# Kernel tuning notes

Hardware: AMD Instinct MI355X
Metric: run time of the kernel (lower is better)

## Reference

```python
import jax, jax.numpy as jnp
import numpy as np

V, D, NH, T_MAX, L, MLP = 50257, 1024, 16, 1024, 12, 4
HD = D // NH
F = D * MLP
B, T = 2, 1024


def setup_inputs() -> dict:
    key = jax.random.key(0)
    ks = jax.random.split(key, 16)
    s = 0.02
    inp = {
        'tokens': jax.random.randint(ks[0], (B, T), 0, V, dtype=jnp.int32),
        'wte': jax.random.normal(ks[1], (V, D), jnp.float32) * s,
        'wpe': jax.random.normal(ks[2], (T_MAX, D), jnp.float32) * s,
        'ln1_w': jnp.ones((L, D)), 'ln1_b': jnp.zeros((L, D)),
        'attn_w': jax.random.normal(ks[3], (L, D, 3 * D), jnp.float32) * s,
        'attn_b': jnp.zeros((L, 3 * D)),
        'aproj_w': jax.random.normal(ks[4], (L, D, D), jnp.float32) * s,
        'aproj_b': jnp.zeros((L, D)),
        'ln2_w': jnp.ones((L, D)), 'ln2_b': jnp.zeros((L, D)),
        'fc_w': jax.random.normal(ks[5], (L, D, F), jnp.float32) * s,
        'fc_b': jnp.zeros((L, F)),
        'proj_w': jax.random.normal(ks[6], (L, F, D), jnp.float32) * s,
        'proj_b': jnp.zeros((L, D)),
        'lnf_w': jnp.ones((D,)), 'lnf_b': jnp.zeros((D,)),
    }
    return inp


def _ln(x, w, b, eps=1e-5):
    m = jnp.mean(x, -1, keepdims=True)
    v = jnp.var(x, -1, keepdims=True)
    return (x - m) * jax.lax.rsqrt(v + eps) * w + b


def _forward(tokens, wte, wpe, ln1_w, ln1_b, attn_w, attn_b, aproj_w, aproj_b,
             ln2_w, ln2_b, fc_w, fc_b, proj_w, proj_b, lnf_w, lnf_b):
    b, t = tokens.shape
    x = wte[tokens] + wpe[:t]  # [B,T,D]
    scale = HD ** -0.5
    causal = jnp.tril(jnp.ones((t, t), bool))  # [T,T]

    def block(x, p):
        l1w, l1b, aw, ab, apw, apb, l2w, l2b, fw, fb, pw, pb = p
        h = _ln(x, l1w, l1b)
        qkv = h @ aw + ab  # [B,T,3D]
        q, k, v = jnp.split(qkv, 3, axis=-1)
        # rearrange 'b t (h n) -> b n t h' with n=NH: last dim is (head_size, n_heads)
        def split_heads(u):
            return u.reshape(b, t, HD, NH).transpose(0, 3, 1, 2)  # [B,NH,T,HD]
        q, k, v = split_heads(q), split_heads(k), split_heads(v)
        scores = jnp.einsum('bnth,bnsh->bnts', q, k) * scale
        scores = jnp.where(causal, scores, -jnp.inf)
        w = jax.nn.softmax(scores, axis=-1)
        att = jnp.einsum('bnts,bnsh->bnth', w, v)
        # rearrange 'b n t h -> b t (n h)'
        att = att.transpose(0, 2, 1, 3).reshape(b, t, D)
        x = x + (att @ apw + apb)
        h2 = _ln(x, l2w, l2b)
        x = x + (jax.nn.gelu(h2 @ fw + fb, approximate=False) @ pw + pb)
        return x, None

    params = (ln1_w, ln1_b, attn_w, attn_b, aproj_w, aproj_b,
              ln2_w, ln2_b, fc_w, fc_b, proj_w, proj_b)
    x, _ = jax.lax.scan(block, x, params)
    x = _ln(x, lnf_w, lnf_b)[:, -1:, :]  # [B,1,D]
    return x @ wte.T  # tied lm_head -> [B,1,V]


def reference(tokens, wte, wpe, ln1_w, ln1_b, attn_w, attn_b, aproj_w, aproj_b,
              ln2_w, ln2_b, fc_w, fc_b, proj_w, proj_b, lnf_w, lnf_b):
    return _forward(tokens, wte, wpe, ln1_w, ln1_b, attn_w, attn_b, aproj_w,
                    aproj_b, ln2_w, ln2_b, fc_w, fc_b, proj_w, proj_b, lnf_w, lnf_b)
```

## Files before the change

kernel.cpp:

```cpp
#include <hip/hip_runtime.h>
#include <cstdint>
#include <math.h>


using u16 = unsigned short;
using bf16x8 = __attribute__((ext_vector_type(8))) short;
using f32x4 = __attribute__((ext_vector_type(4))) float;

#define GLDS16(g, l)                                                        \
  __builtin_amdgcn_global_load_lds(                                         \
      (const __attribute__((address_space(1))) void*)(g),                   \
      (__attribute__((address_space(3))) void*)(l), 16, 0, 0)

__device__ __forceinline__ u16 f2bf(float f) {
  union { float f; unsigned u; } t; t.f = f;
  unsigned r = t.u + 0x7fffu + ((t.u >> 16) & 1u);
  return (u16)(r >> 16);
}

__device__ __forceinline__ float fast_erf(float x) {
  float ax = fabsf(x);
  float t = 1.f / (1.f + 0.3275911f * ax);
  float y = t * (0.254829592f +
            t * (-0.284496736f +
            t * (1.421413741f +
            t * (-1.453152027f +
            t * 1.061405429f))));
  float r = 1.f - y * __expf(-ax * ax);
  return copysignf(r, x);
}

#define DD 1024
#define TTT 1024
#define MR 2048
#define FFF 4096
#define VVV 50257

__global__ __launch_bounds__(256) void k_embed(const int* __restrict__ tokens,
                                               const float* __restrict__ wte,
                                               const float* __restrict__ wpe,
                                               float* __restrict__ x) {
  int m = blockIdx.x, d = threadIdx.x * 4;
  int t = m & (TTT - 1);
  int tok = tokens[m];
  const float4 a = *(const float4*)(wte + (size_t)tok * DD + d);
  const float4 p = *(const float4*)(wpe + (size_t)t * DD + d);
  float4 o; o.x = a.x + p.x; o.y = a.y + p.y; o.z = a.z + p.z; o.w = a.w + p.w;
  *(float4*)(x + (size_t)m * DD + d) = o;
}

__global__ __launch_bounds__(256) void k_ln(const float* __restrict__ x,
                                            const float* __restrict__ w,
                                            const float* __restrict__ b,
                                            u16* __restrict__ out) {
  int m = blockIdx.x, tid = threadIdx.x;
  const float4 v = *(const float4*)(x + (size_t)m * DD + tid * 4);
  float s = v.x + v.y + v.z + v.w;
  float q = v.x * v.x + v.y * v.y + v.z * v.z + v.w * v.w;
#pragma unroll
  for (int off = 1; off < 64; off <<= 1) { s += __shfl_xor(s, off); q += __shfl_xor(q, off); }
  __shared__ float sm[8];
  int wid = tid >> 6;
  if ((tid & 63) == 0) { sm[wid] = s; sm[4 + wid] = q; }
  __syncthreads();
  s = sm[0] + sm[1] + sm[2] + sm[3];
  q = sm[4] + sm[5] + sm[6] + sm[7];
  float mean = s * (1.f / DD);
  float var = q * (1.f / DD) - mean * mean;
  float rs = rsqrtf(var + 1e-5f);
  const float4 wv = *(const float4*)(w + tid * 4);
  const float4 bv = *(const float4*)(b + tid * 4);
  u16 o[4];
  o[0] = f2bf((v.x - mean) * rs * wv.x + bv.x);
  o[1] = f2bf((v.y - mean) * rs * wv.y + bv.y);
  o[2] = f2bf((v.z - mean) * rs * wv.z + bv.z);
  o[3] = f2bf((v.w - mean) * rs * wv.w + bv.w);
  *(uint64_t*)(out + (size_t)m * DD + tid * 4) = *(uint64_t*)o;
}

__global__ __launch_bounds__(256) void k_lnf(const float* __restrict__ x,
                                             const float* __restrict__ w,
                                             const float* __restrict__ b,
                                             float* __restrict__ out) {
  int bb = blockIdx.x, tid = threadIdx.x;
  int m = bb * TTT + (TTT - 1);
  const float4 v = *(const float4*)(x + (size_t)m * DD + tid * 4);
  float s = v.x + v.y + v.z + v.w;
  float q = v.x * v.x + v.y * v.y + v.z * v.z + v.w * v.w;
#pragma unroll
  for (int off = 1; off < 64; off <<= 1) { s += __shfl_xor(s, off); q += __shfl_xor(q, off); }
  __shared__ float sm[8];
  int wid = tid >> 6;
  if ((tid & 63) == 0) { sm[wid] = s; sm[4 + wid] = q; }
  __syncthreads();
  s = sm[0] + sm[1] + sm[2] + sm[3];
  q = sm[4] + sm[5] + sm[6] + sm[7];
  float mean = s * (1.f / DD);
  float var = q * (1.f / DD) - mean * mean;
  float rs = rsqrtf(var + 1e-5f);
  const float4 wv = *(const float4*)(w + tid * 4);
  const float4 bv = *(const float4*)(b + tid * 4);
  float4 o;
  o.x = (v.x - mean) * rs * wv.x + bv.x;
  o.y = (v.y - mean) * rs * wv.y + bv.y;
  o.z = (v.z - mean) * rs * wv.z + bv.z;
  o.w = (v.w - mean) * rs * wv.w + bv.w;
  *(float4*)(out + (size_t)bb * DD + tid * 4) = o;
}

__global__ __launch_bounds__(256) void k_wtrans_all(const float* __restrict__ atw_s,
                                                    const float* __restrict__ apw_s,
                                                    const float* __restrict__ fcw_s,
                                                    const float* __restrict__ pjw_s,
                                                    u16* __restrict__ wt) {
  __shared__ float tile[32][33];
  int id = blockIdx.x;
  const float* W; u16* Wt; int K, N, local, kts;
  if (id < 3072)      { W = atw_s; Wt = wt;           K = 1024; N = 3072; local = id;        kts = 5; }
  else if (id < 4096) { W = apw_s; Wt = wt + 3145728; K = 1024; N = 1024; local = id - 3072; kts = 5; }
  else if (id < 8192) { W = fcw_s; Wt = wt + 4194304; K = 1024; N = 4096; local = id - 4096; kts = 5; }
  else                { W = pjw_s; Wt = wt + 8388608; K = 4096; N = 1024; local = id - 8192; kts = 7; }
  int k0 = (local & ((1 << kts) - 1)) * 32, n0 = (local >> kts) * 32;
  int tx = threadIdx.x & 31, ty = threadIdx.x >> 5;
#pragma unroll
  for (int i = 0; i < 4; ++i)
    tile[ty + i * 8][tx] = W[(size_t)(k0 + ty + i * 8) * N + n0 + tx];
  __syncthreads();
#pragma unroll
  for (int i = 0; i < 4; ++i)
    Wt[(size_t)(n0 + ty + i * 8) * K + k0 + tx] = f2bf(tile[tx][ty + i * 8]);
}

template <int EPI>
__global__ __launch_bounds__(256) void k_gemm(const u16* __restrict__ A,
                                              const u16* __restrict__ Bt,
                                              const float* __restrict__ bias,
                                              u16* __restrict__ outb,
                                              float* __restrict__ xres,
                                              int M, int N, int K, int KC) {
  __shared__ u16 As[2][128 * 64];
  __shared__ u16 Bs[2][128 * 64];
  const int nbx = gridDim.x, nby = gridDim.y;
  const int nwg = nbx * nby * gridDim.z;
  const int orig = blockIdx.x + nbx * (blockIdx.y + nby * blockIdx.z);
  const int qq = nwg >> 3, rr = nwg & 7;
  const int xcd = orig & 7, pos = orig >> 3;
  const int wg = (xcd < rr ? xcd * (qq + 1) : rr * (qq + 1) + (xcd - rr) * qq) + pos;
  const int bx = wg % nbx;
  const int tmpw = wg / nbx;
  const int by = tmpw % nby, bz = tmpw / nby;

  const int tid = threadIdx.x;
  const int lane = tid & 63, wid = tid >> 6;
  const int wr = wid >> 1, wc = wid & 1;
  const int l15 = lane & 15, l4 = lane >> 4;
  const int sx = l15 & 7;
  const int m0 = bx * 128, n0 = by * 128;
  f32x4 acc[4][4] = {};

  const int srow = tid >> 3;
  const int scol = (((tid & 7) ^ ((tid >> 3) & 7)) * 8);
  const int k0beg = bz * KC;
  const int nt = KC >> 6;

  const u16* Ap = A + (size_t)(m0 + srow) * K + scol;
  const u16* Bp = Bt + (size_t)(n0 + srow) * K + scol;

#define STAGE(buf, k0)                                                      \
  {                                                                         \
    _Pragma("unroll")                                                       \
    for (int it = 0; it < 4; ++it) {                                        \
      GLDS16(Ap + (size_t)it * 32 * K + (k0), (char*)As[buf] + it * 4096 + tid * 16); \
      GLDS16(Bp + (size_t)it * 32 * K + (k0), (char*)Bs[buf] + it * 4096 + tid * 16); \
    }                                                                       \
  }

  STAGE(0, k0beg);
  for (int t = 0; t < nt; ++t) {
    if (t + 1 < nt) {
      STAGE((t + 1) & 1, k0beg + (t + 1) * 64);
      asm volatile("s_waitcnt vmcnt(8)" ::: "memory");
    } else {
      asm volatile("s_waitcnt vmcnt(0)" ::: "memory");
    }
    __builtin_amdgcn_sched_barrier(0);
    __builtin_amdgcn_s_barrier();
    __builtin_amdgcn_sched_barrier(0);
    const u16* Ab = As[t & 1];
    const u16* Bb = Bs[t & 1];
#pragma unroll
    for (int ks = 0; ks < 2; ++ks) {
      const int ch = ((ks * 4 + l4) ^ sx) * 8;
      bf16x8 af[4], bfr[4];
#pragma unroll
      for (int i = 0; i < 4; ++i)
        af[i] = *(const bf16x8*)(Ab + (wr * 64 + i * 16 + l15) * 64 + ch);
#pragma unroll
      for (int j = 0; j < 4; ++j)
        bfr[j] = *(const bf16x8*)(Bb + (wc * 64 + j * 16 + l15) * 64 + ch);
      __builtin_amdgcn_s_setprio(1);
#pragma unroll
      for (int i = 0; i < 4; ++i)
#pragma unroll
        for (int j = 0; j < 4; ++j)
          acc[i][j] = __builtin_amdgcn_mfma_f32_16x16x32_bf16(af[i], bfr[j], acc[i][j], 0, 0, 0);
      __builtin_amdgcn_s_setprio(0);
    }
    __builtin_amdgcn_sched_barrier(0);
    __builtin_amdgcn_s_barrier();
    __builtin_amdgcn_sched_barrier(0);
  }
#undef STAGE
#pragma unroll
  for (int j = 0; j < 4; ++j) {
    const int col = n0 + wc * 64 + j * 16 + l15;
    const float bs = (EPI == 3 && bz != 0) ? 0.f : bias[col];
#pragma unroll
    for (int i = 0; i < 4; ++i) {
#pragma unroll
      for (int r = 0; r < 4; ++r) {
        const int row = m0 + wr * 64 + i * 16 + l4 * 4 + r;
        float v = acc[i][j][r] + bs;
        if (EPI == 0) {
          outb[(size_t)row * N + col] = f2bf(v);
        } else if (EPI == 2) {
          float g = 0.5f * v * (1.f + fast_erf(v * 0.70710678118f));
          outb[(size_t)row * N + col] = f2bf(g);
        } else {
          atomicAdd(&xres[(size_t)row * N + col], v);
        }
      }
    }
  }
}

__global__ __launch_bounds__(256) void k_repack(const u16* __restrict__ qkv,
                                                u16* __restrict__ Kb,
                                                u16* __restrict__ Vt) {
  __shared__ u16 tile[16 * 1024];
  const int tid = threadIdx.x;
  const int m0 = blockIdx.x * 16;
  const int part = blockIdx.y + 1;
  const int b = m0 >> 10;
  const int tg0 = m0 & (TTT - 1);
#pragma unroll
  for (int p = 0; p < 8; ++p) {
    int row = p * 2 + (tid >> 7);
    int col8 = (tid & 127) * 8;
    bf16x8 v = *(const bf16x8*)(qkv + (size_t)(m0 + row) * 3072 + part * 1024 + col8);
    int e = col8 ^ (((col8 >> 4) & 7) << 3);
    *(bf16x8*)(tile + row * 1024 + e) = v;
  }
  __syncthreads();
  const int lane = tid & 63, wid = tid >> 6;
  if (part == 1) {
    for (int p = wid; p < 256; p += 4) {
      int t = p >> 4, n = p & 15;
      int e = (lane * 16 + n) ^ ((lane & 7) << 3);
      u16 val = tile[t * 1024 + e];
      Kb[(((size_t)(b * 16 + n)) * TTT + tg0 + t) * 64 + lane] = val;
    }
  } else {
    for (int p = wid; p < 32; p += 4) {
      int n = p >> 1, tc = p & 1;
      int e = (lane * 16 + n) ^ ((lane & 7) << 3);
      u16 val8[8];
#pragma unroll
      for (int k = 0; k < 8; ++k) val8[k] = tile[(tc * 8 + k) * 1024 + e];
      *(bf16x8*)(Vt + (((size_t)(b * 16 + n)) * 64 + lane) * TTT + tg0 + tc * 8) =
          *(bf16x8*)val8;
    }
  }
}

__global__ __launch_bounds__(256) void k_attn(const u16* __restrict__ qkv,
                                              const u16* __restrict__ Kb,
                                              const u16* __restrict__ Vt,
                                              u16* __restrict__ attout) {
  __shared__ u16 Ks[128 * 64];
  __shared__ u16 Vs[64 * 128];
  __shared__ u16 Ps[4][16 * 136];

  const int tid = threadIdx.x;
  const int lane = tid & 63, wid = tid >> 6;
  const int l15 = lane & 15, l4 = lane >> 4;
  const int bn = blockIdx.x;
  const int b = bn >> 4, nh = bn & 15;
  const char* Kg0 = (const char*)(Kb + (size_t)bn * TTT * 64);
  const char* Vg0 = (const char*)(Vt + (size_t)bn * 64 * TTT);

#pragma unroll
  for (int pass = 0; pass < 2; ++pass) {
    const int qtr = pass == 0 ? 15 - (int)blockIdx.y : (int)blockIdx.y;
    const int q0 = qtr * 64;

    const int qrow = q0 + wid * 16 + l15;
    const u16* qsrc = qkv + (size_t)(b * TTT + qrow) * 3072 + nh;
    bf16x8 aq[2];
#pragma unroll
    for (int ks = 0; ks < 2; ++ks) {
      short tmp[8];
#pragma unroll
      for (int j = 0; j < 8; ++j) tmp[j] = (short)qsrc[(ks * 32 + l4 * 8 + j) * 16];
      aq[ks] = *(bf16x8*)tmp;
    }

    float m_run[4], l_part[4];
    f32x4 o[4] = {};
#pragma unroll
    for (int r = 0; r < 4; ++r) { m_run[r] = -1e30f; l_part[r] = 0.f; }

    const int ntk = (qtr >> 1) + 1;
    for (int kt = 0; kt < ntk; ++kt) {
#pragma unroll
      for (int it = 0; it < 4; ++it) {
        int L = it * 4096 + tid * 16;
        int Ls = L ^ (((L >> 7) & 7) << 4);
        GLDS16(Kg0 + (size_t)kt * 16384 + Ls, (char*)Ks + L);
      }
#pragma unroll
      for (int it = 0; it < 4; ++it) {
        int L = it * 4096 + tid * 16;
        int Ls = L ^ (((L >> 8) & 7) << 4);
        int hrow = Ls >> 8, cb = Ls & 255;
        GLDS16(Vg0 + (size_t)hrow * 2048 + kt * 256 + cb, (char*)Vs + L);
      }
      __syncthreads();

      f32x4 sf[8];
#pragma unroll
      for (int cf = 0; cf < 8; ++cf) {
        f32x4 z = {};
#pragma unroll
        for (int ks = 0; ks < 2; ++ks) {
          int P = (cf * 16 + l15) * 128 + (ks * 32 + l4 * 8) * 2;
          bf16x8 kb = *(const bf16x8*)((const char*)Ks + (P ^ (((P >> 7) & 7) << 4)));
          z = __builtin_amdgcn_mfma_f32_16x16x32_bf16(aq[ks], kb, z, 0, 0, 0);
        }
        sf[cf] = z;
      }
      const bool lastkt = (kt == ntk - 1);
#pragma unroll
      for (int cf = 0; cf < 8; ++cf)
#pragma unroll
        for (int r = 0; r < 4; ++r) {
          float s = sf[cf][r] * 0.125f;
          if (lastkt) {
            int kg = kt * 128 + cf * 16 + l15;
            int qg = q0 + wid * 16 + l4 * 4 + r;
            if (kg > qg) s = -1e30f;
          }
          sf[cf][r] = s;
        }
      float fac[4];
#pragma unroll
      for (int r = 0; r < 4; ++r) {
        float tm = sf[0][r];
#pragma unroll
        for (int cf = 1; cf < 8; ++cf) tm = fmaxf(tm, sf[cf][r]);
#pragma unroll
        for (int off = 1; off < 16; off <<= 1) tm = fmaxf(tm, __shfl_xor(tm, off));
        float mnew = fmaxf(m_run[r], tm);
        fac[r] = __expf(m_run[r] - mnew);
        m_run[r] = mnew;
        float ps = 0.f;
#pragma unroll
        for (int cf = 0; cf < 8; ++cf) {
          float p = __expf(sf[cf][r] - mnew);
          sf[cf][r] = p;
          ps += p;
        }
        l_part[r] = l_part[r] * fac[r] + ps;
      }
#pragma unroll
      for (int cf = 0; cf < 8; ++cf)
#pragma unroll
        for (int r = 0; r < 4; ++r)
          Ps[wid][(l4 * 4 + r) * 136 + cf * 16 + l15] = f2bf(sf[cf][r]);
#pragma unroll
      for (int hf = 0; hf < 4; ++hf)
#pragma unroll
        for (int r = 0; r < 4; ++r) o[hf][r] *= fac[r];
      bf16x8 pa[4];
#pragma unroll
      for (int ks = 0; ks < 4; ++ks)
        pa[ks] = *(const bf16x8*)&Ps[wid][l15 * 136 + ks * 32 + l4 * 8];
#pragma unroll
      for (int hf = 0; hf < 4; ++hf) {
#pragma unroll
        for (int ks = 0; ks < 4; ++ks) {
          int P = (hf * 16 + l15) * 256 + (ks * 32 + l4 * 8) * 2;
          bf16x8 vb = *(const bf16x8*)((const char*)Vs + (P ^ (((P >> 8) & 7) << 4)));
          o[hf] = __builtin_amdgcn_mfma_f32_16x16x32_bf16(pa[ks], vb, o[hf], 0, 0, 0);
        }
      }
      __syncthreads();
    }
    float lsum[4];
#pragma unroll
    for (int r = 0; r < 4; ++r) {
      float s = l_part[r];
#pragma unroll
      for (int off = 1; off < 16; off <<= 1) s += __shfl_xor(s, off);
      lsum[r] = s;
    }
#pragma unroll
    for (int hf = 0; hf < 4; ++hf)
#pragma unroll
      for (int r = 0; r < 4; ++r) {
        float val = o[hf][r] / lsum[r];
        size_t row = (size_t)b * TTT + q0 + wid * 16 + l4 * 4 + r;
        attout[row * DD + nh * 64 + hf * 16 + l15] = f2bf(val);
      }
  }
}

__global__ __launch_bounds__(256) void k_head(const float* __restrict__ xlnf,
                                              const float* __restrict__ wte,
                                              float* __restrict__ out) {
  __shared__ float xs[2 * DD];
  int tid = threadIdx.x;
#pragma unroll
  for (int i = 0; i < 2; ++i)
    *(float4*)(xs + i * DD + tid * 4) = *(const float4*)(xlnf + i * DD + tid * 4);
  __syncthreads();
  int wid = tid >> 6, lane = tid & 63;
  for (int v = blockIdx.x * 4 + wid; v < VVV; v += gridDim.x * 4) {
    const float* wr = wte + (size_t)v * DD;
    float a0 = 0.f, a1 = 0.f;
#pragma unroll
    for (int j = 0; j < 4; ++j) {
      const float4 wv = *(const float4*)(wr + lane * 16 + j * 4);
      const float4 x0 = *(const float4*)(xs + lane * 16 + j * 4);
      const float4 x1 = *(const float4*)(xs + DD + lane * 16 + j * 4);
      a0 += wv.x * x0.x + wv.y * x0.y + wv.z * x0.z + wv.w * x0.w;
      a1 += wv.x * x1.x + wv.y * x1.y + wv.z * x1.z + wv.w * x1.w;
    }
#pragma unroll
    for (int off = 1; off < 64; off <<= 1) { a0 += __shfl_xor(a0, off); a1 += __shfl_xor(a1, off); }
    if (lane == 0) { out[v] = a0; out[VVV + v] = a1; }
  }
}

extern "C" void kernel_launch(void* const* d_in, const int* in_sizes, int n_in,
                              void* d_out, int out_size, void* d_ws, size_t ws_size,
                              hipStream_t stream) {
  const int* tokens    = (const int*)d_in[0];
  const float* wte     = (const float*)d_in[1];
  const float* wpe     = (const float*)d_in[2];
  const float* ln1_w   = (const float*)d_in[3];
  const float* ln1_b   = (const float*)d_in[4];
  const float* attn_w  = (const float*)d_in[5];
  const float* attn_b  = (const float*)d_in[6];
  const float* aproj_w = (const float*)d_in[7];
  const float* aproj_b = (const float*)d_in[8];
  const float* ln2_w   = (const float*)d_in[9];
  const float* ln2_b   = (const float*)d_in[10];
  const float* fc_w    = (const float*)d_in[11];
  const float* fc_b    = (const float*)d_in[12];
  const float* proj_w  = (const float*)d_in[13];
  const float* proj_b  = (const float*)d_in[14];
  const float* lnf_w   = (const float*)d_in[15];
  const float* lnf_b   = (const float*)d_in[16];

  char* ws = (char*)d_ws;
  float* x    = (float*)(ws);
  u16* h      = (u16*)(ws + (8u << 20));
  u16* wt     = (u16*)(ws + (12u << 20));
  u16* qkv    = (u16*)(ws + (36u << 20));
  u16* Kb     = (u16*)(ws + (48u << 20));
  u16* Vt     = (u16*)(ws + (52u << 20));
  u16* attb   = (u16*)(ws + (56u << 20));
  u16* mlph   = (u16*)(ws + (36u << 20));
  float* xlnf = (float*)(ws + (60u << 20));
  float* out  = (float*)d_out;

  u16* atw = wt;
  u16* apw = wt + 3145728;
  u16* fcw = wt + 4194304;
  u16* pjw = wt + 8388608;

  k_embed<<<MR, 256, 0, stream>>>(tokens, wte, wpe, x);

  for (int l = 0; l < 12; ++l) {
    k_wtrans_all<<<12288, 256, 0, stream>>>(attn_w + (size_t)l * DD * 3 * DD,
                                            aproj_w + (size_t)l * DD * DD,
                                            fc_w + (size_t)l * DD * FFF,
                                            proj_w + (size_t)l * FFF * DD, wt);
    k_ln<<<MR, 256, 0, stream>>>(x, ln1_w + l * DD, ln1_b + l * DD, h);
    k_gemm<0><<<dim3(16, 24, 1), 256, 0, stream>>>(h, atw, attn_b + (size_t)l * 3 * DD, qkv, nullptr, MR, 3072, 1024, 1024);
    k_repack<<<dim3(128, 2), 256, 0, stream>>>(qkv, Kb, Vt);
    k_attn<<<dim3(32, 8), 256, 0, stream>>>(qkv, Kb, Vt, attb);
    k_gemm<3><<<dim3(16, 8, 2), 256, 0, stream>>>(attb, apw, aproj_b + (size_t)l * DD, nullptr, x, MR, 1024, 1024, 512);
    k_ln<<<MR, 256, 0, stream>>>(x, ln2_w + l * DD, ln2_b + l * DD, h);
    k_gemm<2><<<dim3(16, 32, 1), 256, 0, stream>>>(h, fcw, fc_b + (size_t)l * FFF, mlph, nullptr, MR, 4096, 1024, 1024);
    k_gemm<3><<<dim3(16, 8, 4), 256, 0, stream>>>(mlph, pjw, proj_b + (size_t)l * DD, nullptr, x, MR, 1024, 4096, 1024);
  }
  k_lnf<<<2, 256, 0, stream>>>(x, lnf_w, lnf_b, xlnf);
  k_head<<<512, 256, 0, stream>>>(xlnf, wte, out);
}
```

Before: 2.154 ms.

## Enlarge GEMM tile to 256x128 with 512 threads and fuse final LN into head

The GEMM kernel moves to a 256-row by 128-column tile computed by 8 waves, with staging and the wait count adjusted to match. This raises reuse of each B tile and halves the grid in M. The attention-projection split-K goes from 2 to 4 to keep enough workgroups. Separately, the final layernorm is folded into the LM-head kernel so one launch disappears. Each head block redundantly recomputes the two LN rows, and the visible part does not show whether the wave-to-tile mapping (wr = wid>>1 with 8 waves) covers the whole 256-row tile.

```diff
diff --git a/kernel.cpp b/kernel.cpp
--- a/kernel.cpp
+++ b/kernel.cpp
@@ -78,36 +78,6 @@
   *(uint64_t*)(out + (size_t)m * DD + tid * 4) = *(uint64_t*)o;
 }
 
-__global__ __launch_bounds__(256) void k_lnf(const float* __restrict__ x,
-                                             const float* __restrict__ w,
-                                             const float* __restrict__ b,
-                                             float* __restrict__ out) {
-  int bb = blockIdx.x, tid = threadIdx.x;
-  int m = bb * TTT + (TTT - 1);
-  const float4 v = *(const float4*)(x + (size_t)m * DD + tid * 4);
-  float s = v.x + v.y + v.z + v.w;
-  float q = v.x * v.x + v.y * v.y + v.z * v.z + v.w * v.w;
-#pragma unroll
-  for (int off = 1; off < 64; off <<= 1) { s += __shfl_xor(s, off); q += __shfl_xor(q, off); }
-  __shared__ float sm[8];
-  int wid = tid >> 6;
-  if ((tid & 63) == 0) { sm[wid] = s; sm[4 + wid] = q; }
-  __syncthreads();
-  s = sm[0] + sm[1] + sm[2] + sm[3];
-  q = sm[4] + sm[5] + sm[6] + sm[7];
-  float mean = s * (1.f / DD);
-  float var = q * (1.f / DD) - mean * mean;
-  float rs = rsqrtf(var + 1e-5f);
-  const float4 wv = *(const float4*)(w + tid * 4);
-  const float4 bv = *(const float4*)(b + tid * 4);
-  float4 o;
-  o.x = (v.x - mean) * rs * wv.x + bv.x;
-  o.y = (v.y - mean) * rs * wv.y + bv.y;
-  o.z = (v.z - mean) * rs * wv.z + bv.z;
-  o.w = (v.w - mean) * rs * wv.w + bv.w;
-  *(float4*)(out + (size_t)bb * DD + tid * 4) = o;
-}
-
 __global__ __launch_bounds__(256) void k_wtrans_all(const float* __restrict__ atw_s,
                                                     const float* __restrict__ apw_s,
                                                     const float* __restrict__ fcw_s,
@@ -132,13 +102,13 @@
 }
 
 template <int EPI>
-__global__ __launch_bounds__(256) void k_gemm(const u16* __restrict__ A,
+__global__ __launch_bounds__(512) void k_gemm(const u16* __restrict__ A,
                                               const u16* __restrict__ Bt,
                                               const float* __restrict__ bias,
                                               u16* __restrict__ outb,
                                               float* __restrict__ xres,
                                               int M, int N, int K, int KC) {
-  __shared__ u16 As[2][128 * 64];
+  __shared__ u16 As[2][256 * 64];
   __shared__ u16 Bs[2][128 * 64];
   const int nbx = gridDim.x, nby = gridDim.y;
   const int nwg = nbx * nby * gridDim.z;
@@ -155,11 +125,11 @@
   const int wr = wid >> 1, wc = wid & 1;
   const int l15 = lane & 15, l4 = lane >> 4;
   const int sx = l15 & 7;
-  const int m0 = bx * 128, n0 = by * 128;
+  const int m0 = bx * 256, n0 = by * 128;
   f32x4 acc[4][4] = {};
 
   const int srow = tid >> 3;
-  const int scol = (((tid & 7) ^ ((tid >> 3) & 7)) * 8);
+  const int scol = (((tid & 7) ^ (srow & 7)) * 8);
   const int k0beg = bz * KC;
   const int nt = KC >> 6;
 
@@ -169,17 +139,18 @@
 #define STAGE(buf, k0)                                                      \
   {                                                                         \
     _Pragma("unroll")                                                       \
-    for (int it = 0; it < 4; ++it) {                                        \
-      GLDS16(Ap + (size_t)it * 32 * K + (k0), (char*)As[buf] + it * 4096 + tid * 16); \
-      GLDS16(Bp + (size_t)it * 32 * K + (k0), (char*)Bs[buf] + it * 4096 + tid * 16); \
-    }                                                                       \
+    for (int it = 0; it < 4; ++it)                                          \
+      GLDS16(Ap + (size_t)it * 64 * K + (k0), (char*)As[buf] + it * 8192 + tid * 16); \
+    _Pragma("unroll")                                                       \
+    for (int it = 0; it < 2; ++it)                                          \
+      GLDS16(Bp + (size_t)it * 64 * K + (k0), (char*)Bs[buf] + it * 8192 + tid * 16); \
   }
 
   STAGE(0, k0beg);
   for (int t = 0; t < nt; ++t) {
     if (t + 1 < nt) {
       STAGE((t + 1) & 1, k0beg + (t + 1) * 64);
-      asm volatile("s_waitcnt vmcnt(8)" ::: "memory");
+      asm volatile("s_waitcnt vmcnt(6)" ::: "memory");
     } else {
       asm volatile("s_waitcnt vmcnt(0)" ::: "memory");
     }
@@ -415,16 +386,40 @@
   }
 }
 
-__global__ __launch_bounds__(256) void k_head(const float* __restrict__ xlnf,
+__global__ __launch_bounds__(256) void k_head(const float* __restrict__ x,
+                                              const float* __restrict__ lnf_w,
+                                              const float* __restrict__ lnf_b,
                                               const float* __restrict__ wte,
                                               float* __restrict__ out) {
   __shared__ float xs[2 * DD];
+  __shared__ float sm[8];
   int tid = threadIdx.x;
-#pragma unroll
-  for (int i = 0; i < 2; ++i)
-    *(float4*)(xs + i * DD + tid * 4) = *(const float4*)(xlnf + i * DD + tid * 4);
-  __syncthreads();
   int wid = tid >> 6, lane = tid & 63;
+#pragma unroll
+  for (int bb = 0; bb < 2; ++bb) {
+    int m = bb * TTT + (TTT - 1);
+    const float4 v = *(const float4*)(x + (size_t)m * DD + tid * 4);
+    float s = v.x + v.y + v.z + v.w;
+    float q = v.x * v.x + v.y * v.y + v.z * v.z + v.w * v.w;
+#pragma unroll
+    for (int off = 1; off < 64; off <<= 1) { s += __shfl_xor(s, off); q += __shfl_xor(q, off); }
+    if ((tid & 63) == 0) { sm[wid] = s; sm[4 + wid] = q; }
+    __syncthreads();
+    s = sm[0] + sm[1] + sm[2] + sm[3];
+    q = sm[4] + sm[5] + sm[6] + sm[7];
+    float mean = s * (1.f / DD);
+    float var = q * (1.f / DD) - mean * mean;
+    float rs = rsqrtf(var + 1e-5f);
+    const float4 wv = *(const float4*)(lnf_w + tid * 4);
+    const float4 bv = *(const float4*)(lnf_b + tid * 4);
+    float4 o;
+    o.x = (v.x - mean) * rs * wv.x + bv.x;
+    o.y = (v.y - mean) * rs * wv.y + bv.y;
+    o.z = (v.z - mean) * rs * wv.z + bv.z;
+    o.w = (v.w - mean) * rs * wv.w + bv.w;
+    *(float4*)(xs + bb * DD + tid * 4) = o;
+    __syncthreads();
+  }
   for (int v = blockIdx.x * 4 + wid; v < VVV; v += gridDim.x * 4) {
     const float* wr = wte + (size_t)v * DD;
     float a0 = 0.f, a1 = 0.f;
@@ -472,7 +467,6 @@
   u16* Vt     = (u16*)(ws + (52u << 20));
   u16* attb   = (u16*)(ws + (56u << 20));
   u16* mlph   = (u16*)(ws + (36u << 20));
-  float* xlnf = (float*)(ws + (60u << 20));
   float* out  = (float*)d_out;
 
   u16* atw = wt;
@@ -488,14 +482,13 @@
                                             fc_w + (size_t)l * DD * FFF,
                                             proj_w + (size_t)l * FFF * DD, wt);
     k_ln<<<MR, 256, 0, stream>>>(x, ln1_w + l * DD, ln1_b + l * DD, h);
-    k_gemm<0><<<dim3(16, 24, 1), 256, 0, stream>>>(h, atw, attn_b + (size_t)l * 3 * DD, qkv, nullptr, MR, 3072, 1024, 1024);
+    k_gemm<0><<<dim3(8, 24, 1), 512, 0, stream>>>(h, atw, attn_b + (size_t)l * 3 * DD, qkv, nullptr, MR, 3072, 1024, 1024);
     k_repack<<<dim3(128, 2), 256, 0, stream>>>(qkv, Kb, Vt);
     k_attn<<<dim3(32, 8), 256, 0, stream>>>(qkv, Kb, Vt, attb);
-    k_gemm<3><<<dim3(16, 8, 2), 256, 0, stream>>>(attb, apw, aproj_b + (size_t)l * DD, nullptr, x, MR, 1024, 1024, 512);
+    k_gemm<3><<<dim3(8, 8, 4), 512, 0, stream>>>(attb, apw, aproj_b + (size_t)l * DD, nullptr, x, MR, 1024, 1024, 256);
     k_ln<<<MR, 256, 0, stream>>>(x, ln2_w + l * DD, ln2_b + l * DD, h);
-    k_gemm<2><<<dim3(16, 32, 1), 256, 0, stream>>>(h, fcw, fc_b + (size_t)l * FFF, mlph, nullptr, MR, 4096, 1024, 1024);
-    k_gemm<3><<<dim3(16, 8, 4), 256, 0, stream>>>(mlph, pjw, proj_b + (size_t)l * DD, nullptr, x, MR, 1024, 4096, 1024);
-  }
-  k_lnf<<<2, 256, 0, stream>>>(x, lnf_w, lnf_b, xlnf);
-  k_head<<<512, 256, 0, stream>>>(xlnf, wte, out);
-}
+    k_gemm<2><<<dim3(8, 32, 1), 512, 0, stream>>>(h, fcw, fc_b + (size_t)l * FFF, mlph, nullptr, MR, 4096, 1024, 1024);
+    k_gemm<3><<<dim3(8, 8, 4), 512, 0, stream>>>(mlph, pjw, proj_b + (size_t)l * DD, nullptr, x, MR, 1024, 4096, 1024);
+  }
+  k_head<<<512, 256, 0, stream>>>(x, lnf_w, lnf_b, wte, out);
+}
```

Measured after the change: 2.413 ms. +12.0%, slower.
